# Kernel tuning notes

Measured on AMD Instinct MI355X. Metric: run time of the kernel, lower is better.

The kernel has to match this reference:

```python
import jax, jax.numpy as jnp
import numpy as np

DK, DL, HID = 128, 128, 128  # per init_kwargs: mlp_list=[256,128,128]


def setup_inputs() -> dict:
    key = jax.random.key(0)
    k1, k2, k3, k4, k5 = jax.random.split(key, 5)
    B, K, L = 2, 128, 4096
    inputA = jax.random.normal(k1, (B, K, DK), dtype=jnp.float32)
    inputB = jax.random.normal(k2, (B, L, DL), dtype=jnp.float32)
    # MLP layer 0: Linear(256 -> 128), kaiming-uniform-ish init
    lim1 = 1.0 / np.sqrt(DK + DL)
    W1 = jax.random.uniform(k3, (DK + DL, HID), jnp.float32, -lim1, lim1)
    b1 = jax.random.uniform(k4, (HID,), jnp.float32, -lim1, lim1)
    # scoring Linear(128 -> 1, bias=False)
    lim2 = 1.0 / np.sqrt(HID)
    w2 = jax.random.uniform(k5, (HID,), jnp.float32, -lim2, lim2)
    return {"inputA": inputA, "inputB": inputB, "W1": W1, "b1": b1,
            "w2": w2, "nA": K, "nB": L}


def reference(inputA, inputB, W1, b1, w2, nA, nB):
    # Original: tC = cat([repeat(A), repeat(B)], -1); mlp(tC); linear; softmax(L).
    # Fused-equivalent math: split W1 rows between the A-part and B-part of the
    # concat, so the first Linear is two small matmuls + broadcast add.
    hA = jnp.einsum('bkd,dh->bkh', inputA, W1[:DK])        # (B, K, H)
    hB = jnp.einsum('bld,dh->blh', inputB, W1[DK:])        # (B, L, H)
    h = jax.nn.relu(hA[:, :, None, :] + hB[:, None, :, :] + b1)  # (B, K, L, H)
    scores = jnp.einsum('bklh,h->bkl', h, w2)              # (B, K, L)
    return jax.nn.softmax(scores, axis=2)
```

## Files before the change

kernel.cpp:

```cpp
#include <hip/hip_runtime.h>
#include <hip/hip_fp16.h>
#include <math.h>

constexpr int BB = 2;
constexpr int KK = 128;
constexpr int LL = 4096;
constexpr int DD = 128;
constexpr int HH = 128;

__device__ __forceinline__ float4 ld4(const float* p) {
    return *reinterpret_cast<const float4*>(p);
}

__device__ __forceinline__ __half2 hmax2(__half2 a, __half2 b) {
    unsigned ua = __builtin_bit_cast(unsigned, a);
    unsigned ub = __builtin_bit_cast(unsigned, b);
    unsigned ud;
    asm("v_pk_max_f16 %0, %1, %2" : "=v"(ud) : "v"(ua), "v"(ub));
    return __builtin_bit_cast(__half2, ud);
}

__device__ __forceinline__ uint32_t duph(float x) {
    __half h = __float2half(x);
    unsigned short us = __builtin_bit_cast(unsigned short, h);
    return (uint32_t)us * 0x10001u;
}

__global__ __launch_bounds__(256) void k1_gemm(
    const float* __restrict__ inA, const float* __restrict__ inB,
    const float* __restrict__ W1, const float* __restrict__ b1,
    const float* __restrict__ w2,
    uint32_t* __restrict__ u_dup, uint32_t* __restrict__ w2_dup,
    __half* __restrict__ vT)
{
    __shared__ __align__(16) float sIn[32 * 128];
    __shared__ float sT[128 * 33];

    const int row0 = blockIdx.x * 32;
    const bool isA = (row0 < BB * KK);
    const float* src = isA ? (inA + (size_t)row0 * DD)
                           : (inB + (size_t)(row0 - BB * KK) * DD);
    const float* w   = W1 + (isA ? 0 : DD * HH);

    const int tid = threadIdx.x;

    #pragma unroll
    for (int j = 0; j < 4; ++j) {
        const int idx = tid + 256 * j;
        reinterpret_cast<float4*>(sIn)[idx] =
            reinterpret_cast<const float4*>(src)[idx];
    }
    __syncthreads();

    const int tx = tid & 31;
    const int ty = tid >> 5;

    float accx[4], accy[4], accz[4], accw[4];
    #pragma unroll
    for (int r = 0; r < 4; ++r) { accx[r] = accy[r] = accz[r] = accw[r] = 0.f; }

    for (int d0 = 0; d0 < DD; d0 += 4) {
        float4 w4[4];
        #pragma unroll
        for (int dd = 0; dd < 4; ++dd)
            w4[dd] = ld4(&w[(size_t)(d0 + dd) * HH + tx * 4]);
        float a[4][4];
        #pragma unroll
        for (int r = 0; r < 4; ++r) {
            float4 a4 = ld4(&sIn[(ty * 4 + r) * 128 + d0]);
            a[r][0] = a4.x; a[r][1] = a4.y; a[r][2] = a4.z; a[r][3] = a4.w;
        }
        #pragma unroll
        for (int dd = 0; dd < 4; ++dd) {
            const float4 wv = w4[dd];
            #pragma unroll
            for (int r = 0; r < 4; ++r) {
                const float av = a[r][dd];
                accx[r] = fmaf(av, wv.x, accx[r]);
                accy[r] = fmaf(av, wv.y, accy[r]);
                accz[r] = fmaf(av, wv.z, accz[r]);
                accw[r] = fmaf(av, wv.w, accw[r]);
            }
        }
    }

    if (isA) {
        const float4 bb = ld4(&b1[tx * 4]);
        #pragma unroll
        for (int r = 0; r < 4; ++r) {
            uint4 o;
            o.x = duph(accx[r] + bb.x);
            o.y = duph(accy[r] + bb.y);
            o.z = duph(accz[r] + bb.z);
            o.w = duph(accw[r] + bb.w);
            *reinterpret_cast<uint4*>(&u_dup[(size_t)(row0 + ty * 4 + r) * HH + tx * 4]) = o;
        }
        if (blockIdx.x == 0 && tid < HH) w2_dup[tid] = duph(w2[tid]);
    } else {
        #pragma unroll
        for (int r = 0; r < 4; ++r) {
            const int l = ty * 4 + r;
            sT[(tx * 4 + 0) * 33 + l] = accx[r];
            sT[(tx * 4 + 1) * 33 + l] = accy[r];
            sT[(tx * 4 + 2) * 33 + l] = accz[r];
            sT[(tx * 4 + 3) * 33 + l] = accw[r];
        }
        __syncthreads();
        const int h    = tid >> 1;
        const int half = tid & 1;
        const int rowB = row0 - BB * KK;
        const int bsel = rowB >> 12;
        const int l0   = (rowB & 4095) + half * 16;
        uint32_t o[8];
        #pragma unroll
        for (int i = 0; i < 8; ++i) {
            const float lo = sT[h * 33 + half * 16 + 2 * i];
            const float hi = sT[h * 33 + half * 16 + 2 * i + 1];
            o[i] = __builtin_bit_cast(uint32_t, __floats2half2_rn(lo, hi));
        }
        uint32_t* dst = reinterpret_cast<uint32_t*>(vT) +
                        ((size_t)(bsel * HH + h) * LL + l0) / 2;
        uint4 s0; s0.x = o[0]; s0.y = o[1]; s0.z = o[2]; s0.w = o[3];
        uint4 s1; s1.x = o[4]; s1.y = o[5]; s1.z = o[6]; s1.w = o[7];
        *reinterpret_cast<uint4*>(dst)     = s0;
        *reinterpret_cast<uint4*>(dst + 4) = s1;
    }
}

__global__ __launch_bounds__(256) void k2_score(
    const uint32_t* __restrict__ u_dup, const uint32_t* __restrict__ w2_dup,
    const __half* __restrict__ vT, float* __restrict__ out)
{
    int bi = blockIdx.x;
    const int kt = bi & 31;  bi >>= 5;
    const int lt = bi & 7;   bi >>= 3;
    const int b  = bi;
    const int tid = threadIdx.x;

    const int lp = lt * 256 + tid;
    const uint32_t* vp = reinterpret_cast<const uint32_t*>(vT)
                         + (size_t)b * HH * (LL / 2) + lp;
    const uint32_t* up = u_dup + (size_t)(b * KK + kt * 4) * HH;

    float2 facc[4];
    #pragma unroll
    for (int k = 0; k < 4; ++k) { facc[k].x = 0.f; facc[k].y = 0.f; }

    const __half2 hz = __float2half2_rn(0.f);

    for (int g = 0; g < 8; ++g) {
        __half2 acc[4];
        #pragma unroll
        for (int k = 0; k < 4; ++k) acc[k] = hz;

        #pragma unroll
        for (int c = 0; c < 2; ++c) {
            const int h0 = g * 16 + c * 8;
            uint32_t v[8];
            #pragma unroll
            for (int j = 0; j < 8; ++j)
                v[j] = vp[(size_t)(h0 + j) * (LL / 2)];
            #pragma unroll
            for (int k = 0; k < 4; ++k) {
                #pragma unroll
                for (int j = 0; j < 8; ++j) {
                    const __half2 uu = __builtin_bit_cast(__half2, up[k * HH + h0 + j]);
                    const __half2 ww = __builtin_bit_cast(__half2, w2_dup[h0 + j]);
                    __half2 t = __hadd2(__builtin_bit_cast(__half2, v[j]), uu);
                    acc[k] = __hfma2(hmax2(t, hz), ww, acc[k]);
                }
            }
        }
        #pragma unroll
        for (int k = 0; k < 4; ++k) {
            const float2 f = __half22float2(acc[k]);
            facc[k].x += f.x; facc[k].y += f.y;
        }
    }

    #pragma unroll
    for (int k = 0; k < 4; ++k)
        *reinterpret_cast<float2*>(
            &out[(size_t)(b * KK + kt * 4 + k) * LL + 2 * lp]) = facc[k];
}

__global__ __launch_bounds__(256) void k3_softmax(float* __restrict__ out)
{
    __shared__ float redm[4];
    __shared__ float reds[4];

    const int row = blockIdx.x;
    float* p = out + (size_t)row * LL;
    const int tid = threadIdx.x;

    float4 x[4];
    #pragma unroll
    for (int j = 0; j < 4; ++j)
        x[j] = reinterpret_cast<const float4*>(p)[tid + 256 * j];

    float m = x[0].x;
    #pragma unroll
    for (int j = 0; j < 4; ++j)
        m = fmaxf(m, fmaxf(fmaxf(x[j].x, x[j].y), fmaxf(x[j].z, x[j].w)));
    #pragma unroll
    for (int off = 32; off > 0; off >>= 1)
        m = fmaxf(m, __shfl_xor(m, off, 64));

    const int lane = tid & 63, wv = tid >> 6;
    if (lane == 0) redm[wv] = m;
    __syncthreads();
    m = fmaxf(fmaxf(redm[0], redm[1]), fmaxf(redm[2], redm[3]));

    float s = 0.f;
    #pragma unroll
    for (int j = 0; j < 4; ++j) {
        x[j].x = expf(x[j].x - m); s += x[j].x;
        x[j].y = expf(x[j].y - m); s += x[j].y;
        x[j].z = expf(x[j].z - m); s += x[j].z;
        x[j].w = expf(x[j].w - m); s += x[j].w;
    }
    #pragma unroll
    for (int off = 32; off > 0; off >>= 1)
        s += __shfl_xor(s, off, 64);
    if (lane == 0) reds[wv] = s;
    __syncthreads();
    s = (reds[0] + reds[1]) + (reds[2] + reds[3]);

    const float inv = 1.0f / s;
    #pragma unroll
    for (int j = 0; j < 4; ++j) {
        x[j].x *= inv; x[j].y *= inv; x[j].z *= inv; x[j].w *= inv;
        reinterpret_cast<float4*>(p)[tid + 256 * j] = x[j];
    }
}

extern "C" void kernel_launch(void* const* d_in, const int* in_sizes, int n_in,
                              void* d_out, int out_size, void* d_ws, size_t ws_size,
                              hipStream_t stream)
{
    const float* inA = (const float*)d_in[0];
    const float* inB = (const float*)d_in[1];
    const float* W1  = (const float*)d_in[2];
    const float* b1  = (const float*)d_in[3];
    const float* w2  = (const float*)d_in[4];
    float* out = (float*)d_out;

    uint32_t* u_dup  = (uint32_t*)d_ws;
    uint32_t* w2_dup = (uint32_t*)((char*)d_ws + 128 * 1024);
    __half*   vT     = (__half*)((char*)d_ws + 128 * 1024 + 512);

    hipLaunchKernelGGL(k1_gemm, dim3(264), dim3(256), 0, stream,
                       inA, inB, W1, b1, w2, u_dup, w2_dup, vT);
    hipLaunchKernelGGL(k2_score, dim3(512), dim3(256), 0, stream,
                       u_dup, w2_dup, vT, out);
    hipLaunchKernelGGL(k3_softmax, dim3(BB * KK), dim3(256), 0, stream, out);
}
```

Measured before the change: 33.01 us.

## Halve GEMM tile rows, stage u/w2 in LDS, reorder blocks, widen softmax

The projection kernel now uses 16-row tiles over 528 blocks with a permuted B-row mapping. The score kernel stages the per-block u and w2 vectors in shared memory and reads them with 128-bit loads, loads 16 v rows at once, and puts the L-chunk index innermost in the block order so neighbouring blocks share a k-tile. Softmax uses 1024 threads per row with one float4 each and a two-level reduction. Together these aim to raise occupancy and cut redundant global/scalar loads, at the cost of more register pressure and more sync steps.

```diff
diff --git a/kernel.cpp b/kernel.cpp
--- a/kernel.cpp
+++ b/kernel.cpp
@@ -33,20 +33,27 @@
     uint32_t* __restrict__ u_dup, uint32_t* __restrict__ w2_dup,
     __half* __restrict__ vT)
 {
-    __shared__ __align__(16) float sIn[32 * 128];
-    __shared__ float sT[128 * 33];
-
-    const int row0 = blockIdx.x * 32;
-    const bool isA = (row0 < BB * KK);
+    __shared__ __align__(16) float sIn[16 * 128];
+    __shared__ float sT[128 * 17];
+
+    const int j = blockIdx.x;
+    const bool isA = (j >= 512);
+    int row0;
+    if (isA) {
+        row0 = (j - 512) * 16;
+    } else {
+        const int C = j & 15, s = j >> 4;
+        row0 = (C * 32 + s) * 16;
+    }
     const float* src = isA ? (inA + (size_t)row0 * DD)
-                           : (inB + (size_t)(row0 - BB * KK) * DD);
+                           : (inB + (size_t)row0 * DD);
     const float* w   = W1 + (isA ? 0 : DD * HH);
 
     const int tid = threadIdx.x;
 
     #pragma unroll
-    for (int j = 0; j < 4; ++j) {
-        const int idx = tid + 256 * j;
+    for (int q = 0; q < 2; ++q) {
+        const int idx = tid + 256 * q;
         reinterpret_cast<float4*>(sIn)[idx] =
             reinterpret_cast<const float4*>(src)[idx];
     }
@@ -55,31 +62,32 @@
     const int tx = tid & 31;
     const int ty = tid >> 5;
 
-    float accx[4], accy[4], accz[4], accw[4];
-    #pragma unroll
-    for (int r = 0; r < 4; ++r) { accx[r] = accy[r] = accz[r] = accw[r] = 0.f; }
+    float acc[2][4];
+    #pragma unroll
+    for (int r = 0; r < 2; ++r)
+        #pragma unroll
+        for (int c = 0; c < 4; ++c) acc[r][c] = 0.f;
 
     for (int d0 = 0; d0 < DD; d0 += 4) {
         float4 w4[4];
         #pragma unroll
         for (int dd = 0; dd < 4; ++dd)
             w4[dd] = ld4(&w[(size_t)(d0 + dd) * HH + tx * 4]);
-        float a[4][4];
-        #pragma unroll
-        for (int r = 0; r < 4; ++r) {
-            float4 a4 = ld4(&sIn[(ty * 4 + r) * 128 + d0]);
+        float a[2][4];
+        #pragma unroll
+        for (int r = 0; r < 2; ++r) {
+            float4 a4 = ld4(&sIn[(ty * 2 + r) * 128 + d0]);
             a[r][0] = a4.x; a[r][1] = a4.y; a[r][2] = a4.z; a[r][3] = a4.w;
         }
         #pragma unroll
         for (int dd = 0; dd < 4; ++dd) {
-            const float4 wv = w4[dd];
             #pragma unroll
-            for (int r = 0; r < 4; ++r) {
+            for (int r = 0; r < 2; ++r) {
                 const float av = a[r][dd];
-                accx[r] = fmaf(av, wv.x, accx[r]);
-                accy[r] = fmaf(av, wv.y, accy[r]);
-                accz[r] = fmaf(av, wv.z, accz[r]);
-                accw[r] = fmaf(av, wv.w, accw[r]);
+                acc[r][0] = fmaf(av, w4[dd].x, acc[r][0]);
+                acc[r][1] = fmaf(av, w4[dd].y, acc[r][1]);
+                acc[r][2] = fmaf(av, w4[dd].z, acc[r][2]);
+                acc[r][3] = fmaf(av, w4[dd].w, acc[r][3]);
             }
         }
     }
@@ -87,43 +95,41 @@
     if (isA) {
         const float4 bb = ld4(&b1[tx * 4]);
         #pragma unroll
-        for (int r = 0; r < 4; ++r) {
+        for (int r = 0; r < 2; ++r) {
             uint4 o;
-            o.x = duph(accx[r] + bb.x);
-            o.y = duph(accy[r] + bb.y);
-            o.z = duph(accz[r] + bb.z);
-            o.w = duph(accw[r] + bb.w);
-            *reinterpret_cast<uint4*>(&u_dup[(size_t)(row0 + ty * 4 + r) * HH + tx * 4]) = o;
-        }
-        if (blockIdx.x == 0 && tid < HH) w2_dup[tid] = duph(w2[tid]);
+            o.x = duph(acc[r][0] + bb.x);
+            o.y = duph(acc[r][1] + bb.y);
+            o.z = duph(acc[r][2] + bb.z);
+            o.w = duph(acc[r][3] + bb.w);
+            *reinterpret_cast<uint4*>(
+                &u_dup[(size_t)(row0 + ty * 2 + r) * HH + tx * 4]) = o;
+        }
+        if (j == 512 && tid < HH) w2_dup[tid] = duph(w2[tid]);
     } else {
         #pragma unroll
-        for (int r = 0; r < 4; ++r) {
-            const int l = ty * 4 + r;
-            sT[(tx * 4 + 0) * 33 + l] = accx[r];
-            sT[(tx * 4 + 1) * 33 + l] = accy[r];
-            sT[(tx * 4 + 2) * 33 + l] = accz[r];
-            sT[(tx * 4 + 3) * 33 + l] = accw[r];
+        for (int r = 0; r < 2; ++r) {
+            const int l = ty * 2 + r;
+            sT[(tx * 4 + 0) * 17 + l] = acc[r][0];
+            sT[(tx * 4 + 1) * 17 + l] = acc[r][1];
+            sT[(tx * 4 + 2) * 17 + l] = acc[r][2];
+            sT[(tx * 4 + 3) * 17 + l] = acc[r][3];
         }
         __syncthreads();
         const int h    = tid >> 1;
         const int half = tid & 1;
-        const int rowB = row0 - BB * KK;
-        const int bsel = rowB >> 12;
-        const int l0   = (rowB & 4095) + half * 16;
-        uint32_t o[8];
-        #pragma unroll
-        for (int i = 0; i < 8; ++i) {
-            const float lo = sT[h * 33 + half * 16 + 2 * i];
-            const float hi = sT[h * 33 + half * 16 + 2 * i + 1];
-            o[i] = __builtin_bit_cast(uint32_t, __floats2half2_rn(lo, hi));
+        const int bsel = row0 >> 12;
+        const int l0g  = (row0 & 4095) + half * 8;
+        uint4 o;
+        uint32_t* op = reinterpret_cast<uint32_t*>(&o);
+        #pragma unroll
+        for (int i = 0; i < 4; ++i) {
+            const float lo = sT[h * 17 + half * 8 + 2 * i];
+            const float hi = sT[h * 17 + half * 8 + 2 * i + 1];
+            op[i] = __builtin_bit_cast(uint32_t, __floats2half2_rn(lo, hi));
         }
         uint32_t* dst = reinterpret_cast<uint32_t*>(vT) +
-                        ((size_t)(bsel * HH + h) * LL + l0) / 2;
-        uint4 s0; s0.x = o[0]; s0.y = o[1]; s0.z = o[2]; s0.w = o[3];
-        uint4 s1; s1.x = o[4]; s1.y = o[5]; s1.z = o[6]; s1.w = o[7];
-        *reinterpret_cast<uint4*>(dst)     = s0;
-        *reinterpret_cast<uint4*>(dst + 4) = s1;
+                        (size_t)(bsel * HH + h) * (LL / 2) + l0g / 2;
+        *reinterpret_cast<uint4*>(dst) = o;
     }
 }
 
@@ -131,42 +137,56 @@
     const uint32_t* __restrict__ u_dup, const uint32_t* __restrict__ w2_dup,
     const __half* __restrict__ vT, float* __restrict__ out)
 {
-    int bi = blockIdx.x;
-    const int kt = bi & 31;  bi >>= 5;
-    const int lt = bi & 7;   bi >>= 3;
-    const int b  = bi;
+    __shared__ __align__(16) uint32_t sU[4 * HH];
+    __shared__ __align__(16) uint32_t sW[HH];
+
+    int m = blockIdx.x;
+    const int cb = m & 7;   m >>= 3;
+    const int kt = m & 31;  m >>= 5;
+    const int b  = m;
     const int tid = threadIdx.x;
 
-    const int lp = lt * 256 + tid;
+    if (tid < 128)
+        reinterpret_cast<uint4*>(sU)[tid] =
+            reinterpret_cast<const uint4*>(u_dup + (size_t)(b * KK + kt * 4) * HH)[tid];
+    else if (tid < 160)
+        reinterpret_cast<uint4*>(sW)[tid - 128] =
+            reinterpret_cast<const uint4*>(w2_dup)[tid - 128];
+    __syncthreads();
+
+    const int p = cb * 256 + tid;
     const uint32_t* vp = reinterpret_cast<const uint32_t*>(vT)
-                         + (size_t)b * HH * (LL / 2) + lp;
-    const uint32_t* up = u_dup + (size_t)(b * KK + kt * 4) * HH;
-
+                         + (size_t)b * HH * (LL / 2) + p;
+
+    const __half2 hz = __float2half2_rn(0.f);
     float2 facc[4];
     #pragma unroll
     for (int k = 0; k < 4; ++k) { facc[k].x = 0.f; facc[k].y = 0.f; }
 
-    const __half2 hz = __float2half2_rn(0.f);
-
     for (int g = 0; g < 8; ++g) {
+        const int h0 = g * 16;
+        uint32_t v[16];
+        #pragma unroll
+        for (int jj = 0; jj < 16; ++jj)
+            v[jj] = vp[(size_t)(h0 + jj) * (LL / 2)];
+
         __half2 acc[4];
         #pragma unroll
         for (int k = 0; k < 4; ++k) acc[k] = hz;
 
         #pragma unroll
-        for (int c = 0; c < 2; ++c) {
-            const int h0 = g * 16 + c * 8;
-            uint32_t v[8];
+        for (int k = 0; k < 4; ++k) {
             #pragma unroll
-            for (int j = 0; j < 8; ++j)
-                v[j] = vp[(size_t)(h0 + j) * (LL / 2)];
-            #pragma unroll
-            for (int k = 0; k < 4; ++k) {
+            for (int q = 0; q < 4; ++q) {
+                const uint4 uc = *reinterpret_cast<const uint4*>(&sU[k * HH + h0 + q * 4]);
+                const uint4 wc = *reinterpret_cast<const uint4*>(&sW[h0 + q * 4]);
+                const uint32_t* uq = reinterpret_cast<const uint32_t*>(&uc);
+                const uint32_t* wq = reinterpret_cast<const uint32_t*>(&wc);
                 #pragma unroll
-                for (int j = 0; j < 8; ++j) {
-                    const __half2 uu = __builtin_bit_cast(__half2, up[k * HH + h0 + j]);
-                    const __half2 ww = __builtin_bit_cast(__half2, w2_dup[h0 + j]);
-                    __half2 t = __hadd2(__builtin_bit_cast(__half2, v[j]), uu);
+                for (int jj = 0; jj < 4; ++jj) {
+                    const __half2 uu = __builtin_bit_cast(__half2, uq[jj]);
+                    const __half2 ww = __builtin_bit_cast(__half2, wq[jj]);
+                    __half2 t = __hadd2(__builtin_bit_cast(__half2, v[q * 4 + jj]), uu);
                     acc[k] = __hfma2(hmax2(t, hz), ww, acc[k]);
                 }
             }
@@ -181,57 +201,58 @@
     #pragma unroll
     for (int k = 0; k < 4; ++k)
         *reinterpret_cast<float2*>(
-            &out[(size_t)(b * KK + kt * 4 + k) * LL + 2 * lp]) = facc[k];
-}
-
-__global__ __launch_bounds__(256) void k3_softmax(float* __restrict__ out)
-{
-    __shared__ float redm[4];
-    __shared__ float reds[4];
+            &out[(size_t)(b * KK + kt * 4 + k) * LL + 2 * p]) = facc[k];
+}
+
+__global__ __launch_bounds__(1024) void k3_softmax(float* __restrict__ out)
+{
+    __shared__ float redm[16];
+    __shared__ float reds[16];
 
     const int row = blockIdx.x;
     float* p = out + (size_t)row * LL;
     const int tid = threadIdx.x;
 
-    float4 x[4];
-    #pragma unroll
-    for (int j = 0; j < 4; ++j)
-        x[j] = reinterpret_cast<const float4*>(p)[tid + 256 * j];
-
-    float m = x[0].x;
-    #pragma unroll
-    for (int j = 0; j < 4; ++j)
-        m = fmaxf(m, fmaxf(fmaxf(x[j].x, x[j].y), fmaxf(x[j].z, x[j].w)));
+    float4 x = reinterpret_cast<const float4*>(p)[tid];
+
+    float m = fmaxf(fmaxf(x.x, x.y), fmaxf(x.z, x.w));
     #pragma unroll
     for (int off = 32; off > 0; off >>= 1)
         m = fmaxf(m, __shfl_xor(m, off, 64));
-
     const int lane = tid & 63, wv = tid >> 6;
     if (lane == 0) redm[wv] = m;
     __syncthreads();
-    m = fmaxf(fmaxf(redm[0], redm[1]), fmaxf(redm[2], redm[3]));
-
-    float s = 0.f;
-    #pragma unroll
-    for (int j = 0; j < 4; ++j) {
-        x[j].x = expf(x[j].x - m); s += x[j].x;
-        x[j].y = expf(x[j].y - m); s += x[j].y;
-        x[j].z = expf(x[j].z - m); s += x[j].z;
-        x[j].w = expf(x[j].w - m); s += x[j].w;
-    }
+    if (tid < 16) {
+        float mm = redm[tid];
+        #pragma unroll
+        for (int off = 8; off > 0; off >>= 1)
+            mm = fmaxf(mm, __shfl_xor(mm, off, 64));
+        redm[tid] = mm;
+    }
+    __syncthreads();
+    m = redm[0];
+
+    x.x = expf(x.x - m); x.y = expf(x.y - m);
+    x.z = expf(x.z - m); x.w = expf(x.w - m);
+    float s = (x.x + x.y) + (x.z + x.w);
     #pragma unroll
     for (int off = 32; off > 0; off >>= 1)
         s += __shfl_xor(s, off, 64);
     if (lane == 0) reds[wv] = s;
     __syncthreads();
-    s = (reds[0] + reds[1]) + (reds[2] + reds[3]);
+    if (tid < 16) {
+        float ss = reds[tid];
+        #pragma unroll
+        for (int off = 8; off > 0; off >>= 1)
+            ss += __shfl_xor(ss, off, 64);
+        reds[tid] = ss;
+    }
+    __syncthreads();
+    s = reds[0];
 
     const float inv = 1.0f / s;
-    #pragma unroll
-    for (int j = 0; j < 4; ++j) {
-        x[j].x *= inv; x[j].y *= inv; x[j].z *= inv; x[j].w *= inv;
-        reinterpret_cast<float4*>(p)[tid + 256 * j] = x[j];
-    }
+    x.x *= inv; x.y *= inv; x.z *= inv; x.w *= inv;
+    reinterpret_cast<float4*>(p)[tid] = x;
 }
 
 extern "C" void kernel_launch(void* const* d_in, const int* in_sizes, int n_in,
@@ -249,9 +270,9 @@
     uint32_t* w2_dup = (uint32_t*)((char*)d_ws + 128 * 1024);
     __half*   vT     = (__half*)((char*)d_ws + 128 * 1024 + 512);
 
-    hipLaunchKernelGGL(k1_gemm, dim3(264), dim3(256), 0, stream,
+    hipLaunchKernelGGL(k1_gemm, dim3(528), dim3(256), 0, stream,
                        inA, inB, W1, b1, w2, u_dup, w2_dup, vT);
     hipLaunchKernelGGL(k2_score, dim3(512), dim3(256), 0, stream,
                        u_dup, w2_dup, vT, out);
-    hipLaunchKernelGGL(k3_softmax, dim3(BB * KK), dim3(256), 0, stream, out);
-}
+    hipLaunchKernelGGL(k3_softmax, dim3(BB * KK), dim3(1024), 0, stream, out);
+}
```

After: 33.95 us. 2.8% more time.
